# Performance work log

Hardware: AMD Instinct MI355X
Metric: run time of the kernel (lower is better)

Reference implementation:

```python
import jax, jax.numpy as jnp
import numpy as np


def _resize_hw(x, h, w):
    # PyTorch F.interpolate(mode='bilinear', align_corners=False) == half-pixel
    # bilinear without antialiasing.
    return jax.image.resize(x, x.shape[:-2] + (h, w), method='bilinear', antialias=False)


def _make_char_mask(attn, fore_mask, alpha):
    # attn: [b,26,w_attn] float; fore_mask: [b,1,H,W] int32
    W = fore_mask.shape[-1]
    attn_i = _resize_hw(attn[:, None], 26, W)[:, 0]          # [b,26,W]
    attn_b = (attn_i > alpha).astype(jnp.int32)              # threshold
    single = attn_b[:, :, None, :] * fore_mask               # [b,26,H,W]
    return jnp.concatenate([1 - fore_mask, single], axis=1)  # [b,27,H,W]


def _loss(char_feature, mask, length):
    # char_feature: [b,27,H,W] logits; mask: [b,27,H,W] int; length: [b]
    c = char_feature.shape[1]
    target = jnp.argmax(mask, axis=1)                         # [b,H,W] (first-max, same as torch)
    logp = jax.nn.log_softmax(char_feature, axis=1)
    ce = -jnp.mean(jnp.take_along_axis(logp, target[:, None], axis=1))
    prob = jnp.exp(logp)
    m = mask.astype(prob.dtype)
    smooth = 1.0
    inter = jnp.sum(prob * m, axis=(2, 3))                    # [b,27]
    s1 = jnp.sum(prob, axis=(2, 3))
    s2 = jnp.sum(m, axis=(2, 3))
    score = (2.0 * inter + smooth) / (s1 + s2 + smooth)       # [b,27]
    lens = length - 1                                          # chars per sample
    ch = jnp.arange(c)
    valid = (ch[None, :] >= 1) & (ch[None, :] <= lens[:, None])  # channels 1..len
    per_sample = jnp.sum((1.0 - score) * valid, axis=1) / lens.astype(prob.dtype)
    dice = jnp.mean(per_sample)
    return ce + dice


def setup_inputs() -> dict:
    key = jax.random.key(0)
    k1, k2, k3, k4, k5 = jax.random.split(key, 5)
    b = 512
    return {
        'char_feature_mid': jax.random.normal(k1, (b, 27, 32, 128), dtype=jnp.float32),
        'char_feature_low': jax.random.normal(k2, (b, 27, 16, 64), dtype=jnp.float32),
        'seq1_attention_map': jax.random.uniform(k3, (b, 26, 32), dtype=jnp.float32),
        'fore_mask': jax.random.uniform(k4, (b, 1, 32, 128), dtype=jnp.float32),
        'length': jax.random.randint(k5, (b,), 2, 27),
        'alpha': jnp.float32(0.3),
    }


def reference(char_feature_mid, char_feature_low, seq1_attention_map, fore_mask, length, alpha):
    h_mid, w_mid = char_feature_mid.shape[-2:]
    h_low, w_low = char_feature_low.shape[-2:]
    # clear_noise: zero attention rows at index >= length-1
    keep = jnp.arange(seq1_attention_map.shape[1])[None, :] < (length - 1)[:, None]
    attn = seq1_attention_map * keep[..., None].astype(seq1_attention_map.dtype)
    # low-resolution branch
    fm_low = (_resize_hw(fore_mask, h_low, w_low) >= 0.4).astype(jnp.int32)
    mask_low = _make_char_mask(attn, fm_low, alpha)
    loss_low = _loss(char_feature_low, mask_low, length)
    # middle-resolution branch
    fm_mid = (_resize_hw(fore_mask, h_mid, w_mid) >= 0.4).astype(jnp.int32)
    mask_mid = _make_char_mask(attn, fm_mid, alpha)
    loss_middle = _loss(char_feature_mid, mask_mid, length)
    return ((loss_low, loss_middle), mask_low)
```

## Files before the change

kernel.cpp:

```cpp
#include <hip/hip_runtime.h>
#include <stdint.h>


static __device__ __forceinline__ float wave_reduce_add(float v) {
  v += __shfl_xor(v, 1, 64);
  v += __shfl_xor(v, 2, 64);
  v += __shfl_xor(v, 4, 64);
  v += __shfl_xor(v, 8, 64);
  v += __shfl_xor(v, 16, 64);
  v += __shfl_xor(v, 32, 64);
  return v;
}

static __device__ __forceinline__ uint32_t attn_bits(const float* sattn, float src,
                                                     int lens, float alpha) {
  const int k0 = (int)floorf(src);
  uint32_t bits = 0u;
  if (k0 < 0 || k0 >= 31) {
    const int kk = (k0 < 0) ? 0 : 31;
    for (int c = 0; c < 26; ++c) {
      float v = (c < lens) ? sattn[c * 32 + kk] : 0.0f;
      if (v > alpha) bits |= (1u << c);
    }
  } else {
    const float frac = src - (float)k0;
    const float w1 = frac, w0 = 1.0f - frac;
    for (int c = 0; c < 26; ++c) {
      float v = __fadd_rn(__fmul_rn(w0, sattn[c * 32 + k0]),
                          __fmul_rn(w1, sattn[c * 32 + k0 + 1]));
      v = (c < lens) ? v : 0.0f;
      if (v > alpha) bits |= (1u << c);
    }
  }
  return bits;
}

static __device__ __forceinline__ int fm_low_at(const float* fb, int p) {
  const int y = p >> 6;
  const int x = p & 63;
  const float2* fr = (const float2*)(fb + (size_t)(2 * y) * 128 + 2 * x);
  const float2 f0 = fr[0];
  const float2 f1 = fr[64];
  const float t0 = __fadd_rn(0.5f * f0.x, 0.5f * f1.x);
  const float t1 = __fadd_rn(0.5f * f0.y, 0.5f * f1.y);
  const float fmv = __fadd_rn(0.5f * t0, 0.5f * t1);
  return (fmv >= 0.4f) ? 1 : 0;
}

__global__ __launch_bounds__(256) void prep_kernel(
    const float* __restrict__ attn,
    const float* __restrict__ fore,
    const int* __restrict__ length,
    const float* __restrict__ alpha_p,
    uint32_t* __restrict__ bits_mid,
    uint32_t* __restrict__ bits_low,
    float* __restrict__ acc_mid,
    float* __restrict__ acc_low,
    float* __restrict__ ce) {
  __shared__ float sattn[832];
  __shared__ int colfm_m[128];
  __shared__ int colfm_l[64];
  __shared__ uint32_t sbm[128];
  __shared__ uint32_t sbl[64];
  const int b = blockIdx.x;
  const int t = threadIdx.x;
  const float* fb = fore + (size_t)b * 4096;

  for (int i = t; i < 832; i += 256) sattn[i] = attn[b * 832 + i];
  if (t < 128) colfm_m[t] = 0;
  if (t < 64) colfm_l[t] = 0;
  __syncthreads();

  int pm = 0;
  for (int k = 0; k < 16; ++k) pm += (fb[t + 256 * k] >= 0.4f) ? 1 : 0;
  atomicAdd(&colfm_m[t & 127], pm);
  int pl = 0;
  for (int k = 0; k < 4; ++k) pl += fm_low_at(fb, t + 256 * k);
  atomicAdd(&colfm_l[t & 63], pl);

  const float alpha = alpha_p[0];
  const int lens = length[b] - 1;
  if (t < 128) {
    const uint32_t bm = attn_bits(sattn, 0.25f * (float)t - 0.375f, lens, alpha);
    bits_mid[b * 128 + t] = bm;
    sbm[t] = bm;
  } else if (t < 192) {
    const int x = t - 128;
    const uint32_t bl = attn_bits(sattn, 0.5f * (float)x - 0.25f, lens, alpha);
    bits_low[b * 64 + x] = bl;
    sbl[x] = bl;
  }
  __syncthreads();

  if (t < 54) { acc_mid[(size_t)b * 81 + t] = 0.0f; acc_low[(size_t)b * 81 + t] = 0.0f; }
  if (t >= 64 && t < 91) {
    const int c = t - 64;
    int s2m = 0, s2l = 0;
    if (c == 0) {
      int tm = 0, tl = 0;
      for (int x = 0; x < 128; ++x) tm += colfm_m[x];
      for (int x = 0; x < 64; ++x) tl += colfm_l[x];
      s2m = 4096 - tm;
      s2l = 1024 - tl;
    } else {
      for (int x = 0; x < 128; ++x) s2m += colfm_m[x] * (int)((sbm[x] >> (c - 1)) & 1u);
      for (int x = 0; x < 64; ++x) s2l += colfm_l[x] * (int)((sbl[x] >> (c - 1)) & 1u);
    }
    acc_mid[(size_t)b * 81 + 54 + c] = (float)s2m;
    acc_low[(size_t)b * 81 + 54 + c] = (float)s2l;
  }
  if (b == 0 && t == 63) { ce[0] = 0.0f; ce[1] = 0.0f; }
}

__global__ __launch_bounds__(256, 4) void main_kernel(
    const float* __restrict__ cf_mid,
    const float* __restrict__ cf_low,
    const float* __restrict__ fore,
    float* __restrict__ out,
    const uint32_t* __restrict__ bits_mid,
    const uint32_t* __restrict__ bits_low,
    float* __restrict__ acc_mid,
    float* __restrict__ acc_low,
    float* __restrict__ ce) {
  __shared__ float s_tile[27 * 256];
  __shared__ uint32_t s_bits[128];
  __shared__ float red[4][55];

  const int t = threadIdx.x;
  const int g = blockIdx.x / 5;
  const int r = blockIdx.x % 5;
  const bool low = (r == 4);

  int b, p0, HW;
  const float* cf;
  float* acc;
  if (low) {
    b = g; p0 = 0; HW = 1024;
    cf = cf_low; acc = acc_low;
  } else {
    const int idx = g * 4 + r;
    b = idx >> 2; p0 = (idx & 3) << 10; HW = 4096;
    cf = cf_mid; acc = acc_mid;
  }
  const float* cfb = cf + (size_t)b * 27 * HW;
  const float* fb = fore + (size_t)b * 4096;
  float* mout = out + 2 + (size_t)b * 27 * 1024;

  if (t < (low ? 64 : 128))
    s_bits[t] = (low ? bits_low + (size_t)b * 64 : bits_mid + (size_t)b * 128)[t];

  float inter[27], s1[27];
#pragma unroll
  for (int c = 0; c < 27; ++c) { inter[c] = 0.0f; s1[c] = 0.0f; }
  float cesum = 0.0f;

  const int wv = t >> 6, ln = t & 63;
  const int xmask = low ? 63 : 127;

  for (int j = 0; j < 4; ++j) {
    const int tp0 = p0 + (j << 8);
    for (int c = wv; c < 27; c += 4) {
      const float4 v = *(const float4*)(cfb + (size_t)c * HW + tp0 + 4 * ln);
      *(float4*)&s_tile[c * 256 + 4 * ln] = v;
    }
    __syncthreads();

    const int p = tp0 + t;
    const uint32_t bits = s_bits[t & xmask];
    const int fmw = low ? fm_low_at(fb, p) : ((fb[p] >= 0.4f) ? 1 : 0);
    const int target = fmw ? (int)__ffs(bits) : 0;

    float e[27];
    float z = 0.0f, lt = 0.0f;
#pragma unroll
    for (int c = 0; c < 27; ++c) {
      const float v = s_tile[c * 256 + t];
      lt = (c == target) ? v : lt;
      const float ee = __expf(v);
      e[c] = ee;
      z += ee;
    }
    const float inv = __builtin_amdgcn_rcpf(z);
    cesum += (__logf(z) - lt);

#pragma unroll
    for (int c = 0; c < 27; ++c) {
      const float prob = e[c] * inv;
      s1[c] += prob;
      float mf;
      if (c == 0) mf = (float)(1 - fmw);
      else mf = (float)(((bits >> (c - 1)) & 1u) & (uint32_t)fmw);
      inter[c] = __fmaf_rn(prob, mf, inter[c]);
      if (low) mout[(size_t)c * 1024 + p] = mf;
    }
    __syncthreads();
  }

#pragma unroll
  for (int c = 0; c < 27; ++c) {
    inter[c] = wave_reduce_add(inter[c]);
    s1[c] = wave_reduce_add(s1[c]);
  }
  cesum = wave_reduce_add(cesum);
  if (ln == 0) {
#pragma unroll
    for (int c = 0; c < 27; ++c) {
      red[wv][c] = inter[c];
      red[wv][27 + c] = s1[c];
    }
    red[wv][54] = cesum;
  }
  __syncthreads();
  if (t < 55) {
    const float v = red[0][t] + red[1][t] + red[2][t] + red[3][t];
    if (t == 54) atomicAdd(&ce[low ? 0 : 1], v);
    else atomicAdd(&acc[(size_t)b * 81 + t], v);
  }
}

__global__ __launch_bounds__(256) void final_kernel(
    const float* __restrict__ acc_mid,
    const float* __restrict__ acc_low,
    const float* __restrict__ ce,
    const int* __restrict__ length,
    float* __restrict__ out) {
  const int B = blockIdx.x;
  const float* acc = (B == 0) ? acc_low : acc_mid;
  const float hw = (B == 0) ? 1024.0f : 4096.0f;
  const int t = threadIdx.x;
  float dsum = 0.0f;
  for (int b = t; b < 512; b += 256) {
    const int lens = length[b] - 1;
    const float* a = acc + (size_t)b * 81;
    float d = 0.0f;
    for (int c = 1; c < 27; ++c) {
      const float I = a[c], S1 = a[27 + c], S2 = a[54 + c];
      const float score = (2.0f * I + 1.0f) / (S1 + S2 + 1.0f);
      if (c <= lens) d += (1.0f - score);
    }
    dsum += d / (float)lens;
  }
  __shared__ float red[4];
  const int wave = t >> 6, lane = t & 63;
  dsum = wave_reduce_add(dsum);
  if (lane == 0) red[wave] = dsum;
  __syncthreads();
  if (t == 0) {
    const float dice = red[0] + red[1] + red[2] + red[3];
    out[B] = dice * (1.0f / 512.0f) + ce[B] * (1.0f / (512.0f * hw));
  }
}

extern "C" void kernel_launch(void* const* d_in, const int* in_sizes, int n_in,
                              void* d_out, int out_size, void* d_ws, size_t ws_size,
                              hipStream_t stream) {
  const float* cf_mid = (const float*)d_in[0];
  const float* cf_low = (const float*)d_in[1];
  const float* attn   = (const float*)d_in[2];
  const float* fore   = (const float*)d_in[3];
  const int*   length = (const int*)d_in[4];
  const float* alpha  = (const float*)d_in[5];
  float* out = (float*)d_out;

  uint32_t* bits_mid = (uint32_t*)d_ws;
  uint32_t* bits_low = bits_mid + 512 * 128;
  float* acc_mid = (float*)(bits_low + 512 * 64);
  float* acc_low = acc_mid + 512 * 81;
  float* ce = acc_low + 512 * 81;

  hipLaunchKernelGGL(prep_kernel, dim3(512), dim3(256), 0, stream,
                     attn, fore, length, alpha, bits_mid, bits_low,
                     acc_mid, acc_low, ce);
  hipLaunchKernelGGL(main_kernel, dim3(2560), dim3(256), 0, stream,
                     cf_mid, cf_low, fore, out, bits_mid, bits_low,
                     acc_mid, acc_low, ce);
  hipLaunchKernelGGL(final_kernel, dim3(2), dim3(256), 0, stream,
                     acc_mid, acc_low, ce, length, out);
}
```

Measured before the change: 480.0 us.

## Precompute foreground bitmasks, split mask output into separate kernel, distribute CE accumulation

The prep kernel now packs the thresholded foreground masks into 64-bit ballot words, so the main kernel reads bits instead of reloading fore_mask floats and recomputing the low-resolution resize. Writing the low mask output moves out of main_kernel into a dedicated mask_kernel that uses vectorised stores. The two global CE atomics become per-sample slots in the accumulator arrays, which removes contention. The main kernel also recomputes exp in the second pass instead of holding 27 values in registers, and the launch-bounds occupancy hint is removed. This adds one kernel launch and some extra exp work.

Result: faster. 433.9 us (-9.6%).

```diff
diff --git a/kernel.cpp b/kernel.cpp
--- a/kernel.cpp
+++ b/kernel.cpp
@@ -54,9 +54,10 @@
     const float* __restrict__ alpha_p,
     uint32_t* __restrict__ bits_mid,
     uint32_t* __restrict__ bits_low,
+    unsigned long long* __restrict__ fmm64,
+    unsigned long long* __restrict__ fml64,
     float* __restrict__ acc_mid,
-    float* __restrict__ acc_low,
-    float* __restrict__ ce) {
+    float* __restrict__ acc_low) {
   __shared__ float sattn[832];
   __shared__ int colfm_m[128];
   __shared__ int colfm_l[64];
@@ -64,6 +65,7 @@
   __shared__ uint32_t sbl[64];
   const int b = blockIdx.x;
   const int t = threadIdx.x;
+  const int wv = t >> 6, ln = t & 63;
   const float* fb = fore + (size_t)b * 4096;
 
   for (int i = t; i < 832; i += 256) sattn[i] = attn[b * 832 + i];
@@ -72,10 +74,20 @@
   __syncthreads();
 
   int pm = 0;
-  for (int k = 0; k < 16; ++k) pm += (fb[t + 256 * k] >= 0.4f) ? 1 : 0;
+  for (int k = 0; k < 16; ++k) {
+    const int fm = (fb[t + 256 * k] >= 0.4f) ? 1 : 0;
+    pm += fm;
+    const unsigned long long bal = __ballot(fm);
+    if (ln == 0) fmm64[(size_t)b * 64 + 4 * k + wv] = bal;
+  }
   atomicAdd(&colfm_m[t & 127], pm);
   int pl = 0;
-  for (int k = 0; k < 4; ++k) pl += fm_low_at(fb, t + 256 * k);
+  for (int k = 0; k < 4; ++k) {
+    const int fm = fm_low_at(fb, t + 256 * k);
+    pl += fm;
+    const unsigned long long bal = __ballot(fm);
+    if (ln == 0) fml64[(size_t)b * 16 + 4 * k + wv] = bal;
+  }
   atomicAdd(&colfm_l[t & 63], pl);
 
   const float alpha = alpha_p[0];
@@ -92,7 +104,14 @@
   }
   __syncthreads();
 
-  if (t < 54) { acc_mid[(size_t)b * 81 + t] = 0.0f; acc_low[(size_t)b * 81 + t] = 0.0f; }
+  if (t < 54) {
+    acc_mid[(size_t)b * 82 + t] = 0.0f;
+    acc_low[(size_t)b * 82 + t] = 0.0f;
+  }
+  if (t == 54) {
+    acc_mid[(size_t)b * 82 + 81] = 0.0f;
+    acc_low[(size_t)b * 82 + 81] = 0.0f;
+  }
   if (t >= 64 && t < 91) {
     const int c = t - 64;
     int s2m = 0, s2l = 0;
@@ -106,92 +125,83 @@
       for (int x = 0; x < 128; ++x) s2m += colfm_m[x] * (int)((sbm[x] >> (c - 1)) & 1u);
       for (int x = 0; x < 64; ++x) s2l += colfm_l[x] * (int)((sbl[x] >> (c - 1)) & 1u);
     }
-    acc_mid[(size_t)b * 81 + 54 + c] = (float)s2m;
-    acc_low[(size_t)b * 81 + 54 + c] = (float)s2l;
-  }
-  if (b == 0 && t == 63) { ce[0] = 0.0f; ce[1] = 0.0f; }
-}
-
-__global__ __launch_bounds__(256, 4) void main_kernel(
+    acc_mid[(size_t)b * 82 + 54 + c] = (float)s2m;
+    acc_low[(size_t)b * 82 + 54 + c] = (float)s2l;
+  }
+}
+
+__global__ __launch_bounds__(256) void main_kernel(
     const float* __restrict__ cf_mid,
     const float* __restrict__ cf_low,
-    const float* __restrict__ fore,
-    float* __restrict__ out,
     const uint32_t* __restrict__ bits_mid,
     const uint32_t* __restrict__ bits_low,
+    const unsigned long long* __restrict__ fmm64,
+    const unsigned long long* __restrict__ fml64,
     float* __restrict__ acc_mid,
-    float* __restrict__ acc_low,
-    float* __restrict__ ce) {
+    float* __restrict__ acc_low) {
   __shared__ float s_tile[27 * 256];
   __shared__ uint32_t s_bits[128];
   __shared__ float red[4][55];
 
   const int t = threadIdx.x;
-  const int g = blockIdx.x / 5;
-  const int r = blockIdx.x % 5;
+  const int wv = t >> 6, ln = t & 63;
+  const int g = blockIdx.x / 5, r = blockIdx.x % 5;
   const bool low = (r == 4);
 
-  int b, p0, HW;
+  int b, p0, HW, xmask;
   const float* cf;
   float* acc;
+  const uint32_t* bitsg;
+  const unsigned long long* fmg;
   if (low) {
-    b = g; p0 = 0; HW = 1024;
+    b = g; p0 = 0; HW = 1024; xmask = 63;
     cf = cf_low; acc = acc_low;
+    bitsg = bits_low + (size_t)b * 64;
+    fmg = fml64 + (size_t)b * 16;
   } else {
     const int idx = g * 4 + r;
-    b = idx >> 2; p0 = (idx & 3) << 10; HW = 4096;
+    b = idx >> 2; p0 = (idx & 3) << 10; HW = 4096; xmask = 127;
     cf = cf_mid; acc = acc_mid;
+    bitsg = bits_mid + (size_t)b * 128;
+    fmg = fmm64 + (size_t)b * 64;
   }
   const float* cfb = cf + (size_t)b * 27 * HW;
-  const float* fb = fore + (size_t)b * 4096;
-  float* mout = out + 2 + (size_t)b * 27 * 1024;
-
-  if (t < (low ? 64 : 128))
-    s_bits[t] = (low ? bits_low + (size_t)b * 64 : bits_mid + (size_t)b * 128)[t];
+  if (t <= xmask) s_bits[t] = bitsg[t];
 
   float inter[27], s1[27];
 #pragma unroll
   for (int c = 0; c < 27; ++c) { inter[c] = 0.0f; s1[c] = 0.0f; }
   float cesum = 0.0f;
-
-  const int wv = t >> 6, ln = t & 63;
-  const int xmask = low ? 63 : 127;
 
   for (int j = 0; j < 4; ++j) {
     const int tp0 = p0 + (j << 8);
     for (int c = wv; c < 27; c += 4) {
-      const float4 v = *(const float4*)(cfb + (size_t)c * HW + tp0 + 4 * ln);
-      *(float4*)&s_tile[c * 256 + 4 * ln] = v;
+      *(float4*)&s_tile[c * 256 + 4 * ln] =
+          *(const float4*)(cfb + (size_t)c * HW + tp0 + 4 * ln);
     }
     __syncthreads();
 
-    const int p = tp0 + t;
+    const unsigned long long fw = fmg[(tp0 >> 6) + wv];
+    const int fm = (int)((fw >> ln) & 1ull);
     const uint32_t bits = s_bits[t & xmask];
-    const int fmw = low ? fm_low_at(fb, p) : ((fb[p] >= 0.4f) ? 1 : 0);
-    const int target = fmw ? (int)__ffs(bits) : 0;
-
-    float e[27];
-    float z = 0.0f, lt = 0.0f;
+    const int target = fm ? (int)__ffs(bits) : 0;
+
+    float z = 0.0f;
+#pragma unroll
+    for (int c = 0; c < 27; ++c) z += __expf(s_tile[c * 256 + t]);
+    const float lt = s_tile[target * 256 + t];
+    cesum += __logf(z) - lt;
+    const float inv = __builtin_amdgcn_rcpf(z);
+
+    asm volatile("" ::: "memory");
+
 #pragma unroll
     for (int c = 0; c < 27; ++c) {
-      const float v = s_tile[c * 256 + t];
-      lt = (c == target) ? v : lt;
-      const float ee = __expf(v);
-      e[c] = ee;
-      z += ee;
-    }
-    const float inv = __builtin_amdgcn_rcpf(z);
-    cesum += (__logf(z) - lt);
-
-#pragma unroll
-    for (int c = 0; c < 27; ++c) {
-      const float prob = e[c] * inv;
+      const float prob = __expf(s_tile[c * 256 + t]) * inv;
       s1[c] += prob;
-      float mf;
-      if (c == 0) mf = (float)(1 - fmw);
-      else mf = (float)(((bits >> (c - 1)) & 1u) & (uint32_t)fmw);
+      const float mf = (c == 0) ? (float)(1 - fm)
+                                : (float)(((bits >> (c - 1)) & 1u) & (uint32_t)fm);
       inter[c] = __fmaf_rn(prob, mf, inter[c]);
-      if (low) mout[(size_t)c * 1024 + p] = mf;
     }
     __syncthreads();
   }
@@ -213,25 +223,57 @@
   __syncthreads();
   if (t < 55) {
     const float v = red[0][t] + red[1][t] + red[2][t] + red[3][t];
-    if (t == 54) atomicAdd(&ce[low ? 0 : 1], v);
-    else atomicAdd(&acc[(size_t)b * 81 + t], v);
+    const int slot = (t == 54) ? 81 : t;
+    atomicAdd(&acc[(size_t)b * 82 + slot], v);
+  }
+}
+
+__global__ __launch_bounds__(256) void mask_kernel(
+    const uint32_t* __restrict__ bits_low,
+    const unsigned long long* __restrict__ fml64,
+    float* __restrict__ out) {
+  __shared__ uint32_t sb[64];
+  const int b = blockIdx.x / 3;
+  const int c0 = (blockIdx.x % 3) * 9;
+  const int t = threadIdx.x;
+  if (t < 64) sb[t] = bits_low[(size_t)b * 64 + t];
+  __syncthreads();
+  const int p = 4 * t;
+  const unsigned long long fw = fml64[(size_t)b * 16 + (t >> 4)];
+  uint32_t fmv[4], bb[4];
+#pragma unroll
+  for (int i = 0; i < 4; ++i) {
+    fmv[i] = (uint32_t)((fw >> ((p + i) & 63)) & 1ull);
+    bb[i] = sb[(p + i) & 63];
+  }
+  float* mb = out + 2 + (size_t)b * 27648;
+  for (int cc = 0; cc < 9; ++cc) {
+    const int c = c0 + cc;
+    float v[4];
+#pragma unroll
+    for (int i = 0; i < 4; ++i) {
+      v[i] = (c == 0) ? (float)(1u - fmv[i])
+                      : (float)(((bb[i] >> (c - 1)) & 1u) & fmv[i]);
+    }
+    float* dst = mb + (size_t)c * 1024 + p;
+    *(float2*)dst = make_float2(v[0], v[1]);
+    *(float2*)(dst + 2) = make_float2(v[2], v[3]);
   }
 }
 
 __global__ __launch_bounds__(256) void final_kernel(
     const float* __restrict__ acc_mid,
     const float* __restrict__ acc_low,
-    const float* __restrict__ ce,
     const int* __restrict__ length,
     float* __restrict__ out) {
   const int B = blockIdx.x;
   const float* acc = (B == 0) ? acc_low : acc_mid;
   const float hw = (B == 0) ? 1024.0f : 4096.0f;
   const int t = threadIdx.x;
-  float dsum = 0.0f;
+  float dsum = 0.0f, csum = 0.0f;
   for (int b = t; b < 512; b += 256) {
     const int lens = length[b] - 1;
-    const float* a = acc + (size_t)b * 81;
+    const float* a = acc + (size_t)b * 82;
     float d = 0.0f;
     for (int c = 1; c < 27; ++c) {
       const float I = a[c], S1 = a[27 + c], S2 = a[54 + c];
@@ -239,15 +281,18 @@
       if (c <= lens) d += (1.0f - score);
     }
     dsum += d / (float)lens;
-  }
-  __shared__ float red[4];
+    csum += a[81];
+  }
+  __shared__ float red[4][2];
   const int wave = t >> 6, lane = t & 63;
   dsum = wave_reduce_add(dsum);
-  if (lane == 0) red[wave] = dsum;
+  csum = wave_reduce_add(csum);
+  if (lane == 0) { red[wave][0] = dsum; red[wave][1] = csum; }
   __syncthreads();
   if (t == 0) {
-    const float dice = red[0] + red[1] + red[2] + red[3];
-    out[B] = dice * (1.0f / 512.0f) + ce[B] * (1.0f / (512.0f * hw));
+    const float dice = red[0][0] + red[1][0] + red[2][0] + red[3][0];
+    const float ce = red[0][1] + red[1][1] + red[2][1] + red[3][1];
+    out[B] = dice * (1.0f / 512.0f) + ce * (1.0f / (512.0f * hw));
   }
 }
 
@@ -264,16 +309,19 @@
 
   uint32_t* bits_mid = (uint32_t*)d_ws;
   uint32_t* bits_low = bits_mid + 512 * 128;
-  float* acc_mid = (float*)(bits_low + 512 * 64);
-  float* acc_low = acc_mid + 512 * 81;
-  float* ce = acc_low + 512 * 81;
+  unsigned long long* fmm64 = (unsigned long long*)(bits_low + 512 * 64);
+  unsigned long long* fml64 = fmm64 + 512 * 64;
+  float* acc_mid = (float*)(fml64 + 512 * 16);
+  float* acc_low = acc_mid + 512 * 82;
 
   hipLaunchKernelGGL(prep_kernel, dim3(512), dim3(256), 0, stream,
                      attn, fore, length, alpha, bits_mid, bits_low,
-                     acc_mid, acc_low, ce);
+                     fmm64, fml64, acc_mid, acc_low);
   hipLaunchKernelGGL(main_kernel, dim3(2560), dim3(256), 0, stream,
-                     cf_mid, cf_low, fore, out, bits_mid, bits_low,
-                     acc_mid, acc_low, ce);
+                     cf_mid, cf_low, bits_mid, bits_low, fmm64, fml64,
+                     acc_mid, acc_low);
+  hipLaunchKernelGGL(mask_kernel, dim3(1536), dim3(256), 0, stream,
+                     bits_low, fml64, out);
   hipLaunchKernelGGL(final_kernel, dim3(2), dim3(256), 0, stream,
-                     acc_mid, acc_low, ce, length, out);
-}
+                     acc_mid, acc_low, length, out);
+}
```
